# Optimization experiments

Measured on AMD Instinct MI355X. Metric: run time of the kernel, lower is better.

## Reference

```python
import jax, jax.numpy as jnp
import numpy as np

EMB = 1024
HEAD = 64


def setup_inputs() -> dict:
    key = jax.random.key(0)
    kx, kq, kk, kv = jax.random.split(key, 4)
    x = jax.random.normal(kx, (4, 4096, EMB), dtype=jnp.float32)
    # nn.Linear(emb, head, bias=False): y = x @ W^T; store transposed [emb, head]
    s = 1.0 / np.sqrt(EMB)
    Wq = jax.random.uniform(kq, (EMB, HEAD), jnp.float32, -s, s)
    Wk = jax.random.uniform(kk, (EMB, HEAD), jnp.float32, -s, s)
    Wv = jax.random.uniform(kv, (EMB, HEAD), jnp.float32, -s, s)
    return {"x": x, "Wq": Wq, "Wk": Wk, "Wv": Wv}


def reference(x, Wq, Wk, Wv):
    # x: [B, T, E]; projections -> [B, T, H]
    Q = jnp.einsum("bte,eh->bth", x, Wq)
    K = jnp.einsum("bte,eh->bth", x, Wk)
    V = jnp.einsum("bte,eh->bth", x, Wv)
    scale = 1.0 / np.sqrt(HEAD).astype(np.float32)
    scores = jnp.einsum("bqh,bkh->bqk", Q, K) * scale  # [B, T, T]
    attn = jax.nn.softmax(scores, axis=-1)
    out = jnp.einsum("bqk,bkh->bqh", attn, V)  # [B, T, H]
    return out
```

## Files before the change

kernel.cpp:

```cpp
#include <hip/hip_runtime.h>
#include <hip/hip_bf16.h>

typedef __bf16 bf16x8 __attribute__((ext_vector_type(8)));
typedef float floatx4 __attribute__((ext_vector_type(4)));

#define B_ 4
#define T_ 4096
#define E_ 1024
#define H_ 64
#define NSEG 8
#define SEGLEN (T_ / NSEG)
#define NROWS (B_ * T_)

#define QSCALE 0.18033688011112042f

#if __has_builtin(__builtin_amdgcn_exp2f)
#define EXP2(x) __builtin_amdgcn_exp2f(x)
#else
#define EXP2(x) exp2f(x)
#endif

__device__ __forceinline__ floatx4 mfma16(bf16x8 a, bf16x8 b, floatx4 c) {
  return __builtin_amdgcn_mfma_f32_16x16x32_bf16(a, b, c, 0, 0, 0);
}

#define GLDS16(gp, lp)                                                        \
  __builtin_amdgcn_global_load_lds(                                           \
      (const __attribute__((address_space(1))) void*)(gp),                    \
      (__attribute__((address_space(3))) void*)(lp), 16, 0, 0)

__global__ void prep_wt_k(const float* __restrict__ Wq, const float* __restrict__ Wk,
                          const float* __restrict__ Wv, __bf16* __restrict__ Wfrag) {
  int gid = blockIdx.x * 4 + (threadIdx.x >> 6);
  int lane = threadIdx.x & 63;
  int ch = gid / 24, rem = gid % 24;
  int nt = rem >> 1, half = rem & 1;
  int g = lane >> 4, lm = lane & 15;
  int w = nt >> 2;
  const float* W = (w == 0) ? Wq : (w == 1) ? Wk : Wv;
  float sc = (w == 0) ? QSCALE : 1.0f;
  int h = (nt & 3) * 16 + lm;
  int e0 = ch * 64 + half * 32 + g * 8;
  __bf16* dst = Wfrag + (size_t)gid * 1024 / 2 + lane * 8;
  bf16x8 v;
#pragma unroll
  for (int j = 0; j < 8; j++) v[j] = (__bf16)(W[(size_t)(e0 + j) * H_ + h] * sc);
  *(bf16x8*)dst = v;
}

__global__ void proj_k(
    const float* __restrict__ x, const __bf16* __restrict__ Wfrag,
    __bf16* __restrict__ Qo, __bf16* __restrict__ Ko, __bf16* __restrict__ Vt) {
  __shared__ __align__(16) char sX[8192];
  __shared__ __align__(16) char sW[24576];

  int tid = threadIdx.x;
  int wv = tid >> 6, lane = tid & 63;
  int lm = lane & 15, g = lane >> 4;
  int row_base = blockIdx.x * 32;

  const char* xb = (const char*)x;
  const char* wfb = (const char*)Wfrag;

  int xrow[2], xswz[2];
#pragma unroll
  for (int i = 0; i < 2; i++) {
    int s = i * 256 + tid;
    xrow[i] = s >> 4;
    xswz[i] = ((s & 15) ^ (xrow[i] & 15)) << 4;
  }

  floatx4 acc[2][3];
#pragma unroll
  for (int rg = 0; rg < 2; rg++)
#pragma unroll
    for (int i = 0; i < 3; i++) acc[rg][i] = (floatx4)0.0f;

  for (int ch = 0; ch < 16; ch++) {
#pragma unroll
    for (int i = 0; i < 2; i++)
      GLDS16(xb + (size_t)(row_base + xrow[i]) * 4096 + (size_t)ch * 256 + xswz[i],
             sX + (i * 256 + tid) * 16);
#pragma unroll
    for (int j = 0; j < 6; j++)
      GLDS16(wfb + (size_t)ch * 24576 + j * 4096 + tid * 16,
             sW + j * 4096 + tid * 16);
    __syncthreads();

    bf16x8 a[2][2];
#pragma unroll
    for (int rg = 0; rg < 2; rg++)
#pragma unroll
      for (int ks = 0; ks < 2; ks++) {
        int c0 = ks * 8 + g * 2;
        const char* xp = sX + (rg * 16 + lm) * 256;
        float4 f0 = *(const float4*)(xp + ((c0 ^ lm) << 4));
        float4 f1 = *(const float4*)(xp + (((c0 + 1) ^ lm) << 4));
        a[rg][ks][0] = (__bf16)f0.x; a[rg][ks][1] = (__bf16)f0.y;
        a[rg][ks][2] = (__bf16)f0.z; a[rg][ks][3] = (__bf16)f0.w;
        a[rg][ks][4] = (__bf16)f1.x; a[rg][ks][5] = (__bf16)f1.y;
        a[rg][ks][6] = (__bf16)f1.z; a[rg][ks][7] = (__bf16)f1.w;
      }

    const char* wB = sW + (size_t)(wv * 3 * 2) * 1024 + lane * 16;
#pragma unroll
    for (int i = 0; i < 3; i++) {
      bf16x8 b0 = *(const bf16x8*)(wB + (size_t)(i * 2) * 1024);
      bf16x8 b1 = *(const bf16x8*)(wB + (size_t)(i * 2 + 1) * 1024);
#pragma unroll
      for (int rg = 0; rg < 2; rg++) {
        acc[rg][i] = mfma16(a[rg][0], b0, acc[rg][i]);
        acc[rg][i] = mfma16(a[rg][1], b1, acc[rg][i]);
      }
    }
    __syncthreads();
  }

#pragma unroll
  for (int i = 0; i < 3; i++) {
    int nt = wv * 3 + i;
    int w = nt >> 2;
    int h = (nt & 3) * 16 + lm;
#pragma unroll
    for (int rg = 0; rg < 2; rg++)
#pragma unroll
      for (int r = 0; r < 4; r++) {
        __bf16 v = (__bf16)acc[rg][i][r];
        int rr = row_base + rg * 16 + g * 4 + r;
        if (w == 0)      Qo[(size_t)rr * H_ + h] = v;
        else if (w == 1) Ko[(size_t)rr * H_ + h] = v;
        else {
          int b = rr >> 12, t = rr & (T_ - 1);
          int kin = t & 63;
          int pos = ((kin >> 5) << 5) + (((kin >> 2) & 3) << 3) +
                    (((kin >> 4) & 1) << 2) + (kin & 3);
          Vt[((size_t)b * H_ + h) * T_ + (t & ~63) + pos] = v;
        }
      }
  }
}

__global__ __launch_bounds__(256, 2) void attn_k(
    const __bf16* __restrict__ Q, const __bf16* __restrict__ K,
    const __bf16* __restrict__ Vt, __bf16* __restrict__ Op, float* __restrict__ lp) {
  __shared__ __align__(16) char sK[2 * 8192];
  __shared__ __align__(16) char sV[2 * 8192];

  int qb = blockIdx.x, b = blockIdx.y, seg = blockIdx.z;
  int tid = threadIdx.x, wv = tid >> 6, lane = tid & 63;
  int lm = lane & 15, g = lane >> 4;
  int q0 = qb * 256 + wv * 64;

  const __bf16* Qb = Q + (size_t)b * T_ * H_;
  const char* Kb = (const char*)(K + (size_t)b * T_ * H_);
  const char* Vb = (const char*)(Vt + (size_t)b * H_ * T_);

  bf16x8 qf[4][2];
#pragma unroll
  for (int qi = 0; qi < 4; qi++)
#pragma unroll
    for (int hs = 0; hs < 2; hs++)
      qf[qi][hs] =
          *(const bf16x8*)&Qb[(size_t)(q0 + qi * 16 + lm) * H_ + hs * 32 + g * 8];

  floatx4 o_acc[4][4], o_l[4];
#pragma unroll
  for (int qi = 0; qi < 4; qi++) {
#pragma unroll
    for (int i = 0; i < 4; i++) o_acc[qi][i] = (floatx4)0.0f;
    o_l[qi] = (floatx4)0.0f;
  }

  bf16x8 vone;
#pragma unroll
  for (int j = 0; j < 8; j++) vone[j] = (__bf16)1.0f;

  int s3 = lm & 7;
  int koff[4][2], voff[2][4];
#pragma unroll
  for (int mt = 0; mt < 4; mt++) {
    koff[mt][0] = (mt * 16 + lm) * 128 + ((g ^ s3) << 4);
    koff[mt][1] = (mt * 16 + lm) * 128 + (((g + 4) ^ s3) << 4);
  }
#pragma unroll
  for (int ks = 0; ks < 2; ks++)
#pragma unroll
    for (int nt = 0; nt < 4; nt++)
      voff[ks][nt] = (nt * 16 + lm) * 128 + (((ks * 4 + g) ^ s3) << 4);

  int srow = tid >> 3, schk = tid & 7;
  int swz0 = (schk ^ (srow & 7)) << 4;

#define ATTN_STAGE(buf, k0_)                                                  \
  {                                                                           \
    int off = (buf) * 8192 + tid * 16;                                        \
    GLDS16(Kb + (size_t)(k0_ + srow) * 128 + swz0, sK + off);                 \
    GLDS16(Kb + (size_t)(k0_ + srow + 32) * 128 + swz0, sK + off + 4096);     \
    GLDS16(Vb + (size_t)srow * (T_ * 2) + (size_t)(k0_) * 2 + swz0, sV + off);\
    GLDS16(Vb + (size_t)(srow + 32) * (T_ * 2) + (size_t)(k0_) * 2 + swz0,    \
           sV + off + 4096);                                                  \
  }

  int kbase = seg * SEGLEN;
  ATTN_STAGE(0, kbase);
  __syncthreads();

  for (int t = 0; t < SEGLEN / 64; t++) {
    if (t + 1 < SEGLEN / 64) ATTN_STAGE((t + 1) & 1, kbase + (t + 1) * 64);
    const char* kB = sK + (t & 1) * 8192;
    const char* vB = sV + (t & 1) * 8192;

    floatx4 s_acc[4][4];
#pragma unroll
    for (int mt = 0; mt < 4; mt++)
#pragma unroll
      for (int qi = 0; qi < 4; qi++) s_acc[mt][qi] = (floatx4)0.0f;
#pragma unroll
    for (int mt = 0; mt < 4; mt++) {
      bf16x8 a0 = *(const bf16x8*)(kB + koff[mt][0]);
      bf16x8 a1 = *(const bf16x8*)(kB + koff[mt][1]);
#pragma unroll
      for (int qi = 0; qi < 4; qi++) {
        s_acc[mt][qi] = mfma16(a0, qf[qi][0], s_acc[mt][qi]);
        s_acc[mt][qi] = mfma16(a1, qf[qi][1], s_acc[mt][qi]);
      }
    }

    bf16x8 pa[4][2];
#pragma unroll
    for (int qi = 0; qi < 4; qi++)
#pragma unroll
      for (int mt = 0; mt < 4; mt++)
#pragma unroll
        for (int r = 0; r < 4; r++)
          pa[qi][mt >> 1][(mt & 1) * 4 + r] = (__bf16)EXP2(s_acc[mt][qi][r]);

#pragma unroll
    for (int ks = 0; ks < 2; ks++) {
      bf16x8 bb[4];
#pragma unroll
      for (int nt = 0; nt < 4; nt++) bb[nt] = *(const bf16x8*)(vB + voff[ks][nt]);
#pragma unroll
      for (int qi = 0; qi < 4; qi++) {
#pragma unroll
        for (int nt = 0; nt < 4; nt++)
          o_acc[qi][nt] = mfma16(pa[qi][ks], bb[nt], o_acc[qi][nt]);
        o_l[qi] = mfma16(pa[qi][ks], vone, o_l[qi]);
      }
    }
    __syncthreads();
  }

  size_t rowbase = (size_t)seg * NROWS + (size_t)b * T_ + qb * 256 + wv * 64;
#pragma unroll
  for (int qi = 0; qi < 4; qi++) {
#pragma unroll
    for (int nt = 0; nt < 4; nt++)
#pragma unroll
      for (int r = 0; r < 4; r++)
        Op[(rowbase + qi * 16 + g * 4 + r) * 64 + nt * 16 + lm] =
            (__bf16)o_acc[qi][nt][r];
    if (lm == 0) {
#pragma unroll
      for (int r = 0; r < 4; r++)
        lp[rowbase + qi * 16 + g * 4 + r] = o_l[qi][r];
    }
  }
}

__global__ void combine_k(const __bf16* __restrict__ Op, const float* __restrict__ lp,
                          float* __restrict__ out) {
  int base = (blockIdx.x * 256 + threadIdx.x) * 8;
  int row = base >> 6;
  float L = 0.0f;
  float o[8];
#pragma unroll
  for (int j = 0; j < 8; j++) o[j] = 0.0f;
#pragma unroll
  for (int s = 0; s < NSEG; s++) {
    L += lp[(size_t)s * NROWS + row];
    bf16x8 v = *(const bf16x8*)&Op[(size_t)s * NROWS * 64 + base];
#pragma unroll
    for (int j = 0; j < 8; j++) o[j] += (float)v[j];
  }
  float inv = 1.0f / L;
  float4 r0 = {o[0] * inv, o[1] * inv, o[2] * inv, o[3] * inv};
  float4 r1 = {o[4] * inv, o[5] * inv, o[6] * inv, o[7] * inv};
  *(float4*)&out[base] = r0;
  *(float4*)&out[base + 4] = r1;
}

extern "C" void kernel_launch(void* const* d_in, const int* in_sizes, int n_in,
                              void* d_out, int out_size, void* d_ws, size_t ws_size,
                              hipStream_t stream) {
  const float* x  = (const float*)d_in[0];
  const float* Wq = (const float*)d_in[1];
  const float* Wk = (const float*)d_in[2];
  const float* Wv = (const float*)d_in[3];
  float* out = (float*)d_out;

  char* ws = (char*)d_ws;
  __bf16* Wf  = (__bf16*)(ws);
  __bf16* Qs  = (__bf16*)(ws + 0x60000);
  __bf16* Ks  = (__bf16*)(ws + 0x260000);
  __bf16* Vts = (__bf16*)(ws + 0x460000);
  __bf16* Op  = (__bf16*)(ws + 0x660000);
  float*  lp  = (float*)(ws + 0x1660000);

  prep_wt_k<<<96, 256, 0, stream>>>(Wq, Wk, Wv, Wf);
  proj_k<<<NROWS / 32, 256, 0, stream>>>(x, Wf, Qs, Ks, Vts);
  attn_k<<<dim3(T_ / 256, B_, NSEG), 256, 0, stream>>>(Qs, Ks, Vts, Op, lp);
  combine_k<<<NROWS * 64 / (256 * 8), 256, 0, stream>>>(Op, lp, out);
}
```

Before: 57.64 us.

## Double-buffer x staging in projection and load weight fragments directly from global

The projection kernel now stages x in 256-column chunks (4 chunks instead of 16) into two 32 KB LDS buffers, prefetching the next chunk while computing on the current one. Weight fragments are no longer staged through LDS; each wave reads its B fragments straight from global/L2. This cuts the number of barriers and overlaps global loads with MFMA work. In exchange it uses 64 KB of LDS per block, which may lower occupancy, and relies on cache for the repeated weight reads.

Result: no change. 58.38 us (+1.3%).

```diff
diff --git a/kernel.cpp b/kernel.cpp
--- a/kernel.cpp
+++ b/kernel.cpp
@@ -48,11 +48,10 @@
   *(bf16x8*)dst = v;
 }
 
-__global__ void proj_k(
+__global__ __launch_bounds__(256) void proj_k(
     const float* __restrict__ x, const __bf16* __restrict__ Wfrag,
     __bf16* __restrict__ Qo, __bf16* __restrict__ Ko, __bf16* __restrict__ Vt) {
-  __shared__ __align__(16) char sX[8192];
-  __shared__ __align__(16) char sW[24576];
+  __shared__ __align__(16) char sX[2 * 32768];
 
   int tid = threadIdx.x;
   int wv = tid >> 6, lane = tid & 63;
@@ -60,15 +59,21 @@
   int row_base = blockIdx.x * 32;
 
   const char* xb = (const char*)x;
-  const char* wfb = (const char*)Wfrag;
-
-  int xrow[2], xswz[2];
-#pragma unroll
-  for (int i = 0; i < 2; i++) {
-    int s = i * 256 + tid;
-    xrow[i] = s >> 4;
-    xswz[i] = ((s & 15) ^ (xrow[i] & 15)) << 4;
-  }
+  const char* wfb = (const char*)Wfrag + lane * 16;
+
+  int xr[8], xsw[8];
+#pragma unroll
+  for (int j = 0; j < 8; j++) {
+    int s = j * 256 + tid;
+    xr[j] = s >> 6;
+    xsw[j] = ((s & 63) ^ xr[j]) << 4;
+  }
+
+#define STAGE_X4(buf, CH)                                                     \
+  _Pragma("unroll") for (int j = 0; j < 8; j++)                               \
+      GLDS16(xb + (size_t)(row_base + xr[j]) * 4096 + (size_t)(CH) * 1024 +   \
+                 xsw[j],                                                      \
+             sX + (buf) * 32768 + (j * 256 + tid) * 16);
 
   floatx4 acc[2][3];
 #pragma unroll
@@ -76,42 +81,39 @@
 #pragma unroll
     for (int i = 0; i < 3; i++) acc[rg][i] = (floatx4)0.0f;
 
-  for (int ch = 0; ch < 16; ch++) {
-#pragma unroll
-    for (int i = 0; i < 2; i++)
-      GLDS16(xb + (size_t)(row_base + xrow[i]) * 4096 + (size_t)ch * 256 + xswz[i],
-             sX + (i * 256 + tid) * 16);
-#pragma unroll
-    for (int j = 0; j < 6; j++)
-      GLDS16(wfb + (size_t)ch * 24576 + j * 4096 + tid * 16,
-             sW + j * 4096 + tid * 16);
-    __syncthreads();
-
-    bf16x8 a[2][2];
-#pragma unroll
-    for (int rg = 0; rg < 2; rg++)
-#pragma unroll
-      for (int ks = 0; ks < 2; ks++) {
-        int c0 = ks * 8 + g * 2;
-        const char* xp = sX + (rg * 16 + lm) * 256;
-        float4 f0 = *(const float4*)(xp + ((c0 ^ lm) << 4));
-        float4 f1 = *(const float4*)(xp + (((c0 + 1) ^ lm) << 4));
-        a[rg][ks][0] = (__bf16)f0.x; a[rg][ks][1] = (__bf16)f0.y;
-        a[rg][ks][2] = (__bf16)f0.z; a[rg][ks][3] = (__bf16)f0.w;
-        a[rg][ks][4] = (__bf16)f1.x; a[rg][ks][5] = (__bf16)f1.y;
-        a[rg][ks][6] = (__bf16)f1.z; a[rg][ks][7] = (__bf16)f1.w;
+  STAGE_X4(0, 0);
+  __syncthreads();
+
+  for (int CH = 0; CH < 4; CH++) {
+    if (CH + 1 < 4) STAGE_X4((CH + 1) & 1, CH + 1);
+    const char* xB = sX + (CH & 1) * 32768;
+
+#pragma unroll
+    for (int m = 0; m < 8; m++) {
+      int wgrp = (CH * 4 + (m >> 1)) * 24 + (m & 1);
+      bf16x8 bw[3];
+#pragma unroll
+      for (int i = 0; i < 3; i++)
+        bw[i] = *(const bf16x8*)(wfb + (size_t)(wgrp + (wv * 3 + i) * 2) * 1024);
+
+      bf16x8 a[2];
+#pragma unroll
+      for (int rg = 0; rg < 2; rg++) {
+        int r = rg * 16 + lm;
+        int c0 = m * 8 + g * 2;
+        const char* xp = xB + r * 1024;
+        float4 f0 = *(const float4*)(xp + ((c0 ^ r) << 4));
+        float4 f1 = *(const float4*)(xp + (((c0 + 1) ^ r) << 4));
+        a[rg][0] = (__bf16)f0.x; a[rg][1] = (__bf16)f0.y;
+        a[rg][2] = (__bf16)f0.z; a[rg][3] = (__bf16)f0.w;
+        a[rg][4] = (__bf16)f1.x; a[rg][5] = (__bf16)f1.y;
+        a[rg][6] = (__bf16)f1.z; a[rg][7] = (__bf16)f1.w;
       }
-
-    const char* wB = sW + (size_t)(wv * 3 * 2) * 1024 + lane * 16;
-#pragma unroll
-    for (int i = 0; i < 3; i++) {
-      bf16x8 b0 = *(const bf16x8*)(wB + (size_t)(i * 2) * 1024);
-      bf16x8 b1 = *(const bf16x8*)(wB + (size_t)(i * 2 + 1) * 1024);
-#pragma unroll
-      for (int rg = 0; rg < 2; rg++) {
-        acc[rg][i] = mfma16(a[rg][0], b0, acc[rg][i]);
-        acc[rg][i] = mfma16(a[rg][1], b1, acc[rg][i]);
-      }
+#pragma unroll
+      for (int i = 0; i < 3; i++)
+#pragma unroll
+        for (int rg = 0; rg < 2; rg++)
+          acc[rg][i] = mfma16(a[rg], bw[i], acc[rg][i]);
     }
     __syncthreads();
   }
```
